# Kernel tuning notes

Measured on AMD Instinct MI355X. Metric: run time of the kernel, lower is better.

The kernel has to match this reference:

```python
import jax, jax.numpy as jnp
import numpy as np

N_EMBED = 1024
HEAD_SIZE = 128
B, T = 8, 2048

def setup_inputs() -> dict:
    key = jax.random.key(0)
    kx, kq, kk, kv = jax.random.split(key, 4)
    x = jax.random.normal(kx, (B, T, N_EMBED), dtype=jnp.float32)
    s = N_EMBED ** -0.5
    Wq = jax.random.normal(kq, (N_EMBED, HEAD_SIZE), dtype=jnp.float32) * s
    Wk = jax.random.normal(kk, (N_EMBED, HEAD_SIZE), dtype=jnp.float32) * s
    Wv = jax.random.normal(kv, (N_EMBED, HEAD_SIZE), dtype=jnp.float32) * s
    return {"x": x, "Wq": Wq, "Wk": Wk, "Wv": Wv}

def reference(x, Wq, Wk, Wv):
    # x: [B, T, C]; single causal attention head, eval mode (dropout = identity).
    Bb, Tt, C = x.shape
    q = x @ Wq  # [B, T, H]
    k = x @ Wk  # [B, T, H]
    v = x @ Wv  # [B, T, H]
    # NOTE: original scales by C**-0.5 with C = n_embed (input dim), not head_size.
    wgt = jnp.einsum('bqh,bkh->bqk', q, k) * (C ** -0.5)  # [B, T, T]
    causal = jnp.tril(jnp.ones((Tt, Tt), dtype=bool))
    wgt = jnp.where(causal, wgt, -jnp.inf)
    wgt = jax.nn.softmax(wgt, axis=-1)
    return wgt @ v  # [B, T, H]
```

## Files before the change

kernel.cpp:

```cpp
#include <hip/hip_runtime.h>
#include <hip/hip_bf16.h>

#define B_  8
#define T_  2048
#define C_  1024
#define H_  128

using f32x4  = __attribute__((ext_vector_type(4))) float;
using bf16x8 = __attribute__((ext_vector_type(8))) short;

__device__ __forceinline__ unsigned short f2bf(float f) {
    union { float f; unsigned u; } v; v.f = f;
    unsigned r = v.u + 0x7FFFu + ((v.u >> 16) & 1u);
    return (unsigned short)(r >> 16);
}

#define GLD16(gp, lp) \
    __builtin_amdgcn_global_load_lds((const __attribute__((address_space(1))) void*)(gp), \
                                     (__attribute__((address_space(3))) void*)(lp), 16, 0, 0)

template<int C>
__device__ __forceinline__ float dppf(float v) {
    return __int_as_float(__builtin_amdgcn_update_dpp(0, __float_as_int(v), C, 0xF, 0xF, true));
}
#define DPPRED_MAX(v) { v = fmaxf(v, dppf<0xB1>(v)); v = fmaxf(v, dppf<0x4E>(v)); \
                        v = fmaxf(v, dppf<0x141>(v)); v = fmaxf(v, dppf<0x140>(v)); }
#define DPPRED_SUM(v) { v = v + dppf<0xB1>(v); v = v + dppf<0x4E>(v); \
                        v = v + dppf<0x141>(v); v = v + dppf<0x140>(v); }

__global__ void wconv_kernel(const float* __restrict__ Wq,
                             const float* __restrict__ Wk,
                             const float* __restrict__ Wv,
                             unsigned short* __restrict__ Wt) {
    int id  = blockIdx.x * 256 + threadIdx.x;
    int col = id % 384;
    int k   = id / 384;
    const float* W = (col < 128) ? Wq : ((col < 256) ? Wk : Wv);
    float v = W[k * H_ + (col & 127)];
    if (col < 128) v *= 0.03125f;
    const int kt = k >> 5, sub = (k >> 3) & 3, e = k & 7;
    Wt[(size_t)kt * 12288 + (sub * 384 + col) * 8 + e] = f2bf(v);
}

__launch_bounds__(512, 2)
__global__ void gemm_kernel(const float* __restrict__ x,
                            const unsigned short* __restrict__ Wt,
                            unsigned short* __restrict__ qb,
                            unsigned short* __restrict__ kb,
                            unsigned short* __restrict__ vT) {
    __shared__ __align__(16) unsigned short Bs[2][12288];
    __shared__ __align__(16) unsigned short As[2][2048];

    const int tid  = threadIdx.x;
    const int wave = tid >> 6;
    const int lane = tid & 63;
    const int lo = lane & 15, hi = lane >> 4;
    const int row0 = blockIdx.x * 64;

    const int arow = tid >> 3;
    const int aq   = tid & 7;
    const float* xsrc = x + (size_t)(row0 + arow) * C_ + aq * 4;
    const int aoff = ((aq >> 1) * 64 + arow) * 8 + (aq & 1) * 4;

    const unsigned short* bsrc0 = Wt + (size_t)(wave * 3) * 512 + lane * 8;

    f32x4 acc[4][3];
    #pragma unroll
    for (int rt = 0; rt < 4; ++rt)
        #pragma unroll
        for (int ct = 0; ct < 3; ++ct)
            acc[rt][ct] = f32x4{0.f, 0.f, 0.f, 0.f};

    {
        #pragma unroll
        for (int j = 0; j < 3; ++j)
            GLD16(bsrc0 + j * 512, &Bs[0][(wave * 3 + j) * 512]);
        float4 f = *(const float4*)xsrc;
        unsigned a0 = f2bf(f.x) | ((unsigned)f2bf(f.y) << 16);
        unsigned a1 = f2bf(f.z) | ((unsigned)f2bf(f.w) << 16);
        *(uint2*)&As[0][aoff] = uint2{a0, a1};
    }
    float4 h = *(const float4*)(xsrc + 32);
    __syncthreads();

    for (int k = 0; k < 32; ++k) {
        const int cur = k & 1, nxt = cur ^ 1;

        if (k < 31) {
            const unsigned short* g = bsrc0 + (size_t)(k + 1) * 12288;
            GLD16(g,        &Bs[nxt][(wave * 3) * 512]);
            GLD16(g + 512,  &Bs[nxt][(wave * 3 + 1) * 512]);
            GLD16(g + 1024, &Bs[nxt][(wave * 3 + 2) * 512]);
        }
        float4 g2;
        if (k < 30) g2 = *(const float4*)(xsrc + (k + 2) * 32);

        bf16x8 af[4], bfr[3];
        #pragma unroll
        for (int rt = 0; rt < 4; ++rt)
            af[rt] = *(const bf16x8*)&As[cur][(hi * 64 + rt * 16 + lo) * 8];
        #pragma unroll
        for (int ct = 0; ct < 3; ++ct)
            bfr[ct] = *(const bf16x8*)&Bs[cur][(hi * 384 + wave * 48 + ct * 16 + lo) * 8];

        __builtin_amdgcn_s_setprio(1);
        #pragma unroll
        for (int ct = 0; ct < 3; ++ct)
            #pragma unroll
            for (int rt = 0; rt < 4; ++rt)
                acc[rt][ct] = __builtin_amdgcn_mfma_f32_16x16x32_bf16(af[rt], bfr[ct], acc[rt][ct], 0, 0, 0);
        __builtin_amdgcn_s_setprio(0);

        if (k < 31) {
            unsigned a0 = f2bf(h.x) | ((unsigned)f2bf(h.y) << 16);
            unsigned a1 = f2bf(h.z) | ((unsigned)f2bf(h.w) << 16);
            *(uint2*)&As[nxt][aoff] = uint2{a0, a1};
        }
        __syncthreads();
        h = g2;
    }

    #pragma unroll
    for (int ct = 0; ct < 3; ++ct) {
        int col = wave * 48 + ct * 16 + lo;
        int head = col >> 7;
        int h2 = col & 127;
        #pragma unroll
        for (int rt = 0; rt < 4; ++rt) {
            #pragma unroll
            for (int r = 0; r < 4; ++r) {
                int rg = row0 + rt * 16 + 4 * hi + r;
                unsigned short val = f2bf(acc[rt][ct][r]);
                if (head == 0)      qb[(size_t)rg * H_ + h2] = val;
                else if (head == 1) kb[(size_t)rg * H_ + h2] = val;
                else {
                    int b = rg >> 11, t = rg & (T_ - 1);
                    vT[((size_t)b * H_ + h2) * T_ + t] = val;
                }
            }
        }
    }
}

__launch_bounds__(512, 2)
__global__ void attn1_kernel(const unsigned short* __restrict__ qb,
                             const unsigned short* __restrict__ kb,
                             const unsigned short* __restrict__ vT,
                             float* __restrict__ Opart,
                             float* __restrict__ MLpart) {
    __shared__ unsigned short Ks[64 * 128];
    __shared__ unsigned short Vs[128 * 64];
    __shared__ unsigned short Ps[8][16][72];

    const int tid  = threadIdx.x;
    const int wave = tid >> 6;
    const int lane = tid & 63;
    const int lo = lane & 15, hi = lane >> 4;

    const int bid   = blockIdx.x;
    const int b     = bid & 7;
    const int chunk = (bid >> 3) & 7;
    const int qt    = 7 - (bid >> 6);
    if (chunk > qt) return;

    const int kv_begin = chunk << 8;
    const size_t bT = (size_t)b * T_;
    const int qrow0 = (qt << 8) + wave * 32;

    const int krow = tid >> 3, kcol = (tid & 7) * 2;
    const int vrow = tid >> 2, vcol = (tid & 3) * 2;
    const unsigned short* kgsrc = kb + (bT + krow) * H_ + kcol * 8;
    const unsigned short* vgsrc = vT + ((size_t)b * H_ + vrow) * T_ + vcol * 8;
    unsigned short* kdst0 = &Ks[krow * 128 + ((kcol ^ (krow & 7)) * 8)];
    unsigned short* kdst1 = &Ks[krow * 128 + (((kcol + 1) ^ (krow & 7)) * 8)];
    unsigned short* vdst0 = &Vs[vrow * 64 + ((vcol ^ (vrow & 7)) * 8)];
    unsigned short* vdst1 = &Vs[vrow * 64 + (((vcol + 1) ^ (vrow & 7)) * 8)];

    bf16x8 qf[2][4];
    #pragma unroll
    for (int q2 = 0; q2 < 2; ++q2)
        #pragma unroll
        for (int kc = 0; kc < 4; ++kc)
            qf[q2][kc] = *(const bf16x8*)(qb + (bT + qrow0 + 16 * q2 + lo) * H_ + kc * 32 + 8 * hi);

    float m[2][4], l[2][4];
    f32x4 o[2][8];
    #pragma unroll
    for (int q2 = 0; q2 < 2; ++q2)
        #pragma unroll
        for (int r = 0; r < 4; ++r) { m[q2][r] = -1e30f; l[q2][r] = 0.f; }
    #pragma unroll
    for (int q2 = 0; q2 < 2; ++q2)
        #pragma unroll
        for (int ct = 0; ct < 8; ++ct) o[q2][ct] = f32x4{0.f, 0.f, 0.f, 0.f};

    uint4 kr0 = *(const uint4*)(kgsrc + (size_t)kv_begin * H_);
    uint4 kr1 = *(const uint4*)(kgsrc + (size_t)kv_begin * H_ + 8);
    uint4 vr0 = *(const uint4*)(vgsrc + kv_begin);
    uint4 vr1 = *(const uint4*)(vgsrc + kv_begin + 8);

    for (int t = 0; t < 4; ++t) {
        const int kv0 = kv_begin + t * 64;
        __syncthreads();
        *(uint4*)kdst0 = kr0;
        *(uint4*)kdst1 = kr1;
        *(uint4*)vdst0 = vr0;
        *(uint4*)vdst1 = vr1;
        __syncthreads();
        if (t < 3) {
            const int kvn = kv0 + 64;
            kr0 = *(const uint4*)(kgsrc + (size_t)kvn * H_);
            kr1 = *(const uint4*)(kgsrc + (size_t)kvn * H_ + 8);
            vr0 = *(const uint4*)(vgsrc + kvn);
            vr1 = *(const uint4*)(vgsrc + kvn + 8);
        }
        if (kv0 > qrow0 + 31) continue;

        f32x4 s[2][4];
        #pragma unroll
        for (int q2 = 0; q2 < 2; ++q2)
            #pragma unroll
            for (int ct4 = 0; ct4 < 4; ++ct4) s[q2][ct4] = f32x4{0.f, 0.f, 0.f, 0.f};
        __builtin_amdgcn_s_setprio(1);
        #pragma unroll
        for (int ct4 = 0; ct4 < 4; ++ct4) {
            const int row = ct4 * 16 + lo;
            #pragma unroll
            for (int kc = 0; kc < 4; ++kc) {
                bf16x8 kf = *(const bf16x8*)&Ks[row * 128 + (((kc * 4 + hi) ^ (row & 7)) * 8)];
                s[0][ct4] = __builtin_amdgcn_mfma_f32_16x16x32_bf16(qf[0][kc], kf, s[0][ct4], 0, 0, 0);
                s[1][ct4] = __builtin_amdgcn_mfma_f32_16x16x32_bf16(qf[1][kc], kf, s[1][ct4], 0, 0, 0);
            }
        }
        __builtin_amdgcn_s_setprio(0);

        if (kv0 + 63 >= qrow0) {
            #pragma unroll
            for (int q2 = 0; q2 < 2; ++q2)
                #pragma unroll
                for (int ct4 = 0; ct4 < 4; ++ct4)
                    #pragma unroll
                    for (int r = 0; r < 4; ++r)
                        if (kv0 + ct4 * 16 + lo > qrow0 + 16 * q2 + 4 * hi + r)
                            s[q2][ct4][r] = -1e30f;
        }

        float alpha[2][4];
        #pragma unroll
        for (int q2 = 0; q2 < 2; ++q2) {
            #pragma unroll
            for (int r = 0; r < 4; ++r) {
                float pm = fmaxf(fmaxf(s[q2][0][r], s[q2][1][r]), fmaxf(s[q2][2][r], s[q2][3][r]));
                DPPRED_MAX(pm);
                float mn = fmaxf(m[q2][r], pm);
                alpha[q2][r] = __expf(m[q2][r] - mn);
                m[q2][r] = mn;
                #pragma unroll
                for (int ct4 = 0; ct4 < 4; ++ct4) s[q2][ct4][r] = __expf(s[q2][ct4][r] - mn);
                float rs = (s[q2][0][r] + s[q2][1][r]) + (s[q2][2][r] + s[q2][3][r]);
                DPPRED_SUM(rs);
                l[q2][r] = l[q2][r] * alpha[q2][r] + rs;
            }
        }
        #pragma unroll
        for (int q2 = 0; q2 < 2; ++q2)
            #pragma unroll
            for (int ct = 0; ct < 8; ++ct)
                #pragma unroll
                for (int r = 0; r < 4; ++r) o[q2][ct][r] *= alpha[q2][r];

        bf16x8 pa[2][2];
        #pragma unroll
        for (int q2 = 0; q2 < 2; ++q2) {
            #pragma unroll
            for (int ct4 = 0; ct4 < 4; ++ct4)
                #pragma unroll
                for (int r = 0; r < 4; ++r)
                    Ps[wave][4 * hi + r][ct4 * 16 + lo] = f2bf(s[q2][ct4][r]);
            pa[q2][0] = *(const bf16x8*)&Ps[wave][lo][8 * hi];
            pa[q2][1] = *(const bf16x8*)&Ps[wave][lo][32 + 8 * hi];
        }

        __builtin_amdgcn_s_setprio(1);
        #pragma unroll
        for (int ct = 0; ct < 8; ++ct) {
            const int row = ct * 16 + lo;
            #pragma unroll
            for (int half = 0; half < 2; ++half) {
                bf16x8 vf = *(const bf16x8*)&Vs[row * 64 + (((half * 4 + hi) ^ (row & 7)) * 8)];
                o[0][ct] = __builtin_amdgcn_mfma_f32_16x16x32_bf16(pa[0][half], vf, o[0][ct], 0, 0, 0);
                o[1][ct] = __builtin_amdgcn_mfma_f32_16x16x32_bf16(pa[1][half], vf, o[1][ct], 0, 0, 0);
            }
        }
        __builtin_amdgcn_s_setprio(0);
    }

    const int slot = b * 36 + ((qt * (qt + 1)) >> 1) + chunk;
    float* op = Opart + (size_t)slot * 32768 + (size_t)(wave * 32) * 128;
    #pragma unroll
    for (int q2 = 0; q2 < 2; ++q2)
        #pragma unroll
        for (int ct = 0; ct < 8; ++ct)
            #pragma unroll
            for (int r = 0; r < 4; ++r)
                op[(16 * q2 + 4 * hi + r) * 128 + ct * 16 + lo] = o[q2][ct][r];
    if (lo == 0) {
        #pragma unroll
        for (int q2 = 0; q2 < 2; ++q2)
            #pragma unroll
            for (int r = 0; r < 4; ++r) {
                int base = slot * 512 + (wave * 32 + 16 * q2 + 4 * hi + r) * 2;
                MLpart[base]     = m[q2][r];
                MLpart[base + 1] = l[q2][r];
            }
    }
}

__launch_bounds__(128)
__global__ void attn2_kernel(const float* __restrict__ Opart,
                             const float* __restrict__ MLpart,
                             float* __restrict__ out) {
    const int bid = blockIdx.x;
    const int b   = bid & 7;
    const int qt  = (bid >> 3) & 7;
    const int sub = bid >> 6;
    const int nch = qt + 1;
    const int slot0 = b * 36 + ((qt * (qt + 1)) >> 1);

    const int tid  = threadIdx.x;
    const int row  = tid >> 2;
    const int h0   = (tid & 3) * 32;
    const int srow = sub * 32 + row;

    float M = -1e30f;
    for (int c = 0; c < nch; ++c)
        M = fmaxf(M, MLpart[(slot0 + c) * 512 + srow * 2]);
    float L = 0.f;
    for (int c = 0; c < nch; ++c) {
        float mc = MLpart[(slot0 + c) * 512 + srow * 2];
        float lc = MLpart[(slot0 + c) * 512 + srow * 2 + 1];
        L += lc * __expf(mc - M);
    }

    float4 acc[8];
    #pragma unroll
    for (int j = 0; j < 8; ++j) acc[j] = float4{0.f, 0.f, 0.f, 0.f};
    for (int c = 0; c < nch; ++c) {
        float wc = __expf(MLpart[(slot0 + c) * 512 + srow * 2] - M);
        const float4* src = (const float4*)(Opart + (size_t)(slot0 + c) * 32768 + (size_t)srow * 128 + h0);
        #pragma unroll
        for (int j = 0; j < 8; ++j) {
            float4 v = src[j];
            acc[j].x += wc * v.x; acc[j].y += wc * v.y;
            acc[j].z += wc * v.z; acc[j].w += wc * v.w;
        }
    }
    float inv = 1.f / L;
    float4* dst = (float4*)(out + ((size_t)b * T_ + qt * 256 + srow) * H_ + h0);
    #pragma unroll
    for (int j = 0; j < 8; ++j) {
        float4 v = acc[j];
        dst[j] = float4{v.x * inv, v.y * inv, v.z * inv, v.w * inv};
    }
}

extern "C" void kernel_launch(void* const* d_in, const int* in_sizes, int n_in,
                              void* d_out, int out_size, void* d_ws, size_t ws_size,
                              hipStream_t stream) {
    const float* x  = (const float*)d_in[0];
    const float* Wq = (const float*)d_in[1];
    const float* Wk = (const float*)d_in[2];
    const float* Wv = (const float*)d_in[3];
    float* out = (float*)d_out;

    char* ws = (char*)d_ws;
    unsigned short* Wt  = (unsigned short*)ws;
    unsigned short* qbf = (unsigned short*)(ws + (size_t)384 * 1024 * 2);
    unsigned short* kbf = qbf + (size_t)B_ * T_ * H_;
    unsigned short* vTf = kbf + (size_t)B_ * T_ * H_;
    float* Opart  = (float*)(vTf + (size_t)B_ * T_ * H_);
    float* MLpart = (float*)((char*)Opart + (size_t)288 * 32768 * 4);

    wconv_kernel<<<(384 * 1024) / 256, 256, 0, stream>>>(Wq, Wk, Wv, Wt);
    gemm_kernel<<<B_ * T_ / 64, 512, 0, stream>>>(x, Wt, qbf, kbf, vTf);
    attn1_kernel<<<512, 512, 0, stream>>>(qbf, kbf, vTf, Opart, MLpart);
    attn2_kernel<<<512, 128, 0, stream>>>(Opart, MLpart, out);
}
```

Before: 92.60 us.

## Triple-buffer QKV projection GEMM with explicit vmcnt-based prefetch pipeline

```diff
diff --git a/kernel.cpp b/kernel.cpp
--- a/kernel.cpp
+++ b/kernel.cpp
@@ -42,14 +42,14 @@
     Wt[(size_t)kt * 12288 + (sub * 384 + col) * 8 + e] = f2bf(v);
 }
 
-__launch_bounds__(512, 2)
+__launch_bounds__(512)
 __global__ void gemm_kernel(const float* __restrict__ x,
                             const unsigned short* __restrict__ Wt,
                             unsigned short* __restrict__ qb,
                             unsigned short* __restrict__ kb,
                             unsigned short* __restrict__ vT) {
-    __shared__ __align__(16) unsigned short Bs[2][12288];
-    __shared__ __align__(16) unsigned short As[2][2048];
+    __shared__ __align__(16) unsigned short Bs[3][12288];
+    __shared__ __align__(16) unsigned short As[3][2048];
 
     const int tid  = threadIdx.x;
     const int wave = tid >> 6;
@@ -62,7 +62,8 @@
     const float* xsrc = x + (size_t)(row0 + arow) * C_ + aq * 4;
     const int aoff = ((aq >> 1) * 64 + arow) * 8 + (aq & 1) * 4;
 
-    const unsigned short* bsrc0 = Wt + (size_t)(wave * 3) * 512 + lane * 8;
+    const unsigned short* bsrc = Wt + (size_t)(wave * 3) * 512 + lane * 8;
+    const int bdst = (wave * 3) * 512;
 
     f32x4 acc[4][3];
     #pragma unroll
@@ -71,29 +72,38 @@
         for (int ct = 0; ct < 3; ++ct)
             acc[rt][ct] = f32x4{0.f, 0.f, 0.f, 0.f};
 
+    f32x4 h0, hA, hB, hn;
+
+    asm volatile("global_load_dwordx4 %0, %1, off" : "=v"(h0) : "v"(xsrc));
+    #pragma unroll
+    for (int j = 0; j < 3; ++j) GLD16(bsrc + j * 512, &Bs[0][bdst + j * 512]);
+    asm volatile("global_load_dwordx4 %0, %1, off" : "=v"(hA) : "v"(xsrc + 32));
+    #pragma unroll
+    for (int j = 0; j < 3; ++j) GLD16(bsrc + 12288 + j * 512, &Bs[1][bdst + j * 512]);
+    asm volatile("global_load_dwordx4 %0, %1, off" : "=v"(hB) : "v"(xsrc + 64));
+
+    asm volatile("s_waitcnt vmcnt(8)" : "+v"(h0) :: "memory");
     {
-        #pragma unroll
-        for (int j = 0; j < 3; ++j)
-            GLD16(bsrc0 + j * 512, &Bs[0][(wave * 3 + j) * 512]);
-        float4 f = *(const float4*)xsrc;
-        unsigned a0 = f2bf(f.x) | ((unsigned)f2bf(f.y) << 16);
-        unsigned a1 = f2bf(f.z) | ((unsigned)f2bf(f.w) << 16);
+        unsigned a0 = f2bf(h0.x) | ((unsigned)f2bf(h0.y) << 16);
+        unsigned a1 = f2bf(h0.z) | ((unsigned)f2bf(h0.w) << 16);
         *(uint2*)&As[0][aoff] = uint2{a0, a1};
     }
-    float4 h = *(const float4*)(xsrc + 32);
-    __syncthreads();
-
-    for (int k = 0; k < 32; ++k) {
-        const int cur = k & 1, nxt = cur ^ 1;
-
-        if (k < 31) {
-            const unsigned short* g = bsrc0 + (size_t)(k + 1) * 12288;
-            GLD16(g,        &Bs[nxt][(wave * 3) * 512]);
-            GLD16(g + 512,  &Bs[nxt][(wave * 3 + 1) * 512]);
-            GLD16(g + 1024, &Bs[nxt][(wave * 3 + 2) * 512]);
-        }
-        float4 g2;
-        if (k < 30) g2 = *(const float4*)(xsrc + (k + 2) * 32);
+    asm volatile("s_waitcnt vmcnt(5) lgkmcnt(0)" ::: "memory");
+    __builtin_amdgcn_sched_barrier(0);
+    __builtin_amdgcn_s_barrier();
+    __builtin_amdgcn_sched_barrier(0);
+
+    int cur = 0, wr = 2, awr = 1;
+    for (int t = 0; t < 32; ++t) {
+        {
+            const int ktI = (t + 2 < 31) ? t + 2 : 31;
+            const unsigned short* g = bsrc + (size_t)ktI * 12288;
+            GLD16(g,        &Bs[wr][bdst]);
+            GLD16(g + 512,  &Bs[wr][bdst + 512]);
+            GLD16(g + 1024, &Bs[wr][bdst + 1024]);
+            const int kx = (t + 3 < 31) ? t + 3 : 31;
+            asm volatile("global_load_dwordx4 %0, %1, off" : "=v"(hn) : "v"(xsrc + kx * 32));
+        }
 
         bf16x8 af[4], bfr[3];
         #pragma unroll
@@ -111,13 +121,22 @@
                 acc[rt][ct] = __builtin_amdgcn_mfma_f32_16x16x32_bf16(af[rt], bfr[ct], acc[rt][ct], 0, 0, 0);
         __builtin_amdgcn_s_setprio(0);
 
-        if (k < 31) {
-            unsigned a0 = f2bf(h.x) | ((unsigned)f2bf(h.y) << 16);
-            unsigned a1 = f2bf(h.z) | ((unsigned)f2bf(h.w) << 16);
-            *(uint2*)&As[nxt][aoff] = uint2{a0, a1};
-        }
-        __syncthreads();
-        h = g2;
+        asm volatile("s_waitcnt vmcnt(8)" : "+v"(hA) :: "memory");
+        {
+            unsigned a0 = f2bf(hA.x) | ((unsigned)f2bf(hA.y) << 16);
+            unsigned a1 = f2bf(hA.z) | ((unsigned)f2bf(hA.w) << 16);
+            *(uint2*)&As[awr][aoff] = uint2{a0, a1};
+        }
+        hA = hB; hB = hn;
+
+        asm volatile("s_waitcnt vmcnt(5) lgkmcnt(0)" ::: "memory");
+        __builtin_amdgcn_sched_barrier(0);
+        __builtin_amdgcn_s_barrier();
+        __builtin_amdgcn_sched_barrier(0);
+
+        cur = (cur == 2) ? 0 : cur + 1;
+        wr  = (wr  == 2) ? 0 : wr  + 1;
+        awr = (awr == 2) ? 0 : awr + 1;
     }
 
     #pragma unroll
```

New measurement: 92.56 us. About the same (-0.0%).
